# Optimization experiments

Hardware: AMD Instinct MI355X
Metric: run time of the kernel (lower is better)

The kernel has to match this reference:

```python
import jax, jax.numpy as jnp
import numpy as np

B, IN, OUT, K = 2048, 1024, 1024, 20


def setup_inputs() -> dict:
    key = jax.random.key(0)
    k1, k2 = jax.random.split(key)
    x = jax.random.normal(k1, (B, IN), dtype=jnp.float32)
    # per-output, per-input spline coefficients: (out_features, in_features, num_knots)
    W = jax.random.normal(k2, (OUT, IN, K), dtype=jnp.float32) * 0.1
    # evenly spaced knot grid on [-2, 2] (linspace)
    knots = jnp.linspace(-2.0, 2.0, K, dtype=jnp.float32)
    return {"x": x, "W": W, "knots": knots}


def reference(x, W, knots):
    # RBF spline basis shared across all output features (this is the fusion
    # the original per-output Python loop misses):
    # basis[b, i, k] = exp(-0.5 * ((x[b, i] - knots[k]) / h)^2)
    h = knots[1] - knots[0]  # uniform knot spacing -> RBF bandwidth
    basis = jnp.exp(-0.5 * jnp.square((x[:, :, None] - knots) / h))  # (B, IN, K)
    # Each SplineLayer o computes sum_{i,k} W[o,i,k] * basis[b,i,k]; the
    # KANBlock concatenates the OUT scalars -> a single einsum.
    return jnp.einsum("bik,oik->bo", basis, W)  # (B, OUT)
```

## Files before the change

### kernel.cpp

```cpp
#include <hip/hip_runtime.h>

#define B_DIM 2048
#define IN_DIM 1024
#define OUT_DIM 1024
#define K_KNOTS 20
#define KR (IN_DIM * K_KNOTS)
#define TM 128
#define TN 128
#define BK 64
#define KSPLIT 4
#define KPB (KR / KSPLIT)
#define OUT_ELEMS (B_DIM * OUT_DIM)
#define MT_TILES (B_DIM / TM)
#define NT_TILES (OUT_DIM / TN)
#define GEMM_BLOCKS (MT_TILES * NT_TILES * KSPLIT)

#define NB_PAIRS (B_DIM * IN_DIM * K_KNOTS / 2)
#define NB_BASIS_BLK (NB_PAIRS / 256)
#define NW4 (OUT_DIM * KR / 8)
#define NB_W_BLK (NW4 / 256)

typedef __bf16 bf16x8 __attribute__((ext_vector_type(8)));
typedef float  f32x4  __attribute__((ext_vector_type(4)));

__device__ __forceinline__ unsigned short f2bf(float f) {
    unsigned int u = __float_as_uint(f);
    unsigned int r = u + 0x7fffu + ((u >> 16) & 1u);
    return (unsigned short)(r >> 16);
}

__device__ __forceinline__ unsigned int pack2(float lo, float hi) {
    return (unsigned int)f2bf(lo) | ((unsigned int)f2bf(hi) << 16);
}

__device__ __forceinline__ void async_load16(const void* g, void* l) {
    __builtin_amdgcn_global_load_lds(
        (const __attribute__((address_space(1))) void*)g,
        (__attribute__((address_space(3))) void*)l,
        16, 0, 0);
}

__global__ void zero_out_kernel(float* out) {
    int idx = (blockIdx.x * 256 + threadIdx.x) * 4;
    float4 z = {0.f, 0.f, 0.f, 0.f};
    *(float4*)(out + idx) = z;
}

__global__ void prep_kernel(const float* __restrict__ x,
                            const float4* __restrict__ Wsrc,
                            const float* __restrict__ knots,
                            unsigned int* __restrict__ basis_out,
                            uint4* __restrict__ w_out) {
    if (blockIdx.x < NB_BASIS_BLK) {
        unsigned int n = blockIdx.x * 256 + threadIdx.x;
        unsigned int p  = n % 10u;
        unsigned int bi = n / 10u;
        float xv   = x[bi];
        float invh = 1.0f / (knots[1] - knots[0]);
        float t0 = knots[2 * p], t1 = knots[2 * p + 1];
        float d0 = (xv - t0) * invh;
        float d1 = (xv - t1) * invh;
        float v0 = __expf(-0.5f * d0 * d0);
        float v1 = __expf(-0.5f * d1 * d1);
        basis_out[n] = pack2(v0, v1);
    } else {
        unsigned int t = (blockIdx.x - NB_BASIS_BLK) * 256 + threadIdx.x;
        float4 a = Wsrc[2 * t];
        float4 b = Wsrc[2 * t + 1];
        uint4 o;
        o.x = pack2(a.x, a.y);
        o.y = pack2(a.z, a.w);
        o.z = pack2(b.x, b.y);
        o.w = pack2(b.z, b.w);
        w_out[t] = o;
    }
}

template <int KS, bool ATOMIC>
__global__ void __launch_bounds__(256)
kan_gemm(const unsigned short* __restrict__ Ab,
         const unsigned short* __restrict__ Bb,
         float* __restrict__ out) {
    __shared__ __align__(16) unsigned short As[TM * BK];
    __shared__ __align__(16) unsigned short Bs[TN * BK];

    const int KPBk = KR / KS;
    const int id   = blockIdx.x;
    const int xcd  = id & 7;
    const int ord  = id >> 3;
    const int mt   = xcd * 2 + (ord & 1);
    const int nt   = (ord >> 1) & (NT_TILES - 1);
    const int z    = ord >> (1 + 3);
    const int m0 = mt * TM;
    const int n0 = nt * TN;
    const int k0 = z * KPBk;

    const int tid  = threadIdx.x;
    const int wave = tid >> 6;
    const int lane = tid & 63;
    const int wm = wave & 1;
    const int wn = wave >> 1;

    const int srow = lane >> 3;
    const int scol = ((lane & 7) ^ srow) * 8;

    f32x4 acc[4][4];
#pragma unroll
    for (int i = 0; i < 4; ++i)
#pragma unroll
        for (int j = 0; j < 4; ++j) acc[i][j] = (f32x4){0.f, 0.f, 0.f, 0.f};

    for (int kt = 0; kt < KPBk; kt += BK) {
        const int kb = k0 + kt;
        __syncthreads();
#pragma unroll
        for (int c = 0; c < 4; ++c) {
            const int chunk = wave * 4 + c;
            const int r = chunk * 8 + srow;
            async_load16(Ab + (size_t)(m0 + r) * KR + kb + scol, &As[chunk * 512]);
            async_load16(Bb + (size_t)(n0 + r) * KR + kb + scol, &Bs[chunk * 512]);
        }
        __syncthreads();

        const int quad = lane >> 4;
        const int r15  = lane & 15;
        const int r7   = lane & 7;
#pragma unroll
        for (int s = 0; s < 2; ++s) {
            const int cg = s * 4 + quad;
            const int xo = (cg ^ r7) * 8;
            bf16x8 af[4], bfv[4];
#pragma unroll
            for (int i = 0; i < 4; ++i) {
                af[i]  = *(const bf16x8*)&As[(wm * 64 + i * 16 + r15) * BK + xo];
                bfv[i] = *(const bf16x8*)&Bs[(wn * 64 + i * 16 + r15) * BK + xo];
            }
#pragma unroll
            for (int i = 0; i < 4; ++i)
#pragma unroll
                for (int j = 0; j < 4; ++j)
                    acc[i][j] = __builtin_amdgcn_mfma_f32_16x16x32_bf16(
                        af[i], bfv[j], acc[i][j], 0, 0, 0);
        }
    }

    float* dst = ATOMIC ? out : out + (size_t)z * OUT_ELEMS;
    const int quad = lane >> 4;
    const int col  = lane & 15;
#pragma unroll
    for (int i = 0; i < 4; ++i)
#pragma unroll
        for (int j = 0; j < 4; ++j)
#pragma unroll
            for (int r = 0; r < 4; ++r) {
                const int row = m0 + wm * 64 + i * 16 + quad * 4 + r;
                const int c   = n0 + wn * 64 + j * 16 + col;
                if (ATOMIC)
                    atomicAdd(&dst[(size_t)row * OUT_DIM + c], acc[i][j][r]);
                else
                    dst[(size_t)row * OUT_DIM + c] = acc[i][j][r];
            }
}

template <int KS>
__global__ void kan_reduce(const float* __restrict__ part, float* __restrict__ out) {
    const int idx = (blockIdx.x * 256 + threadIdx.x) * 4;
    f32x4 s = *(const f32x4*)(part + idx);
#pragma unroll
    for (int z = 1; z < KS; ++z)
        s += *(const f32x4*)(part + (size_t)z * OUT_ELEMS + idx);
    *(f32x4*)(out + idx) = s;
}

__global__ void kan_fallback(const float* __restrict__ x,
                             const float* __restrict__ W,
                             const float* __restrict__ knots,
                             float* __restrict__ out) {
    __shared__ float basis[256 * K_KNOTS];
    const int b = blockIdx.x;
    const int o = blockIdx.y * blockDim.x + threadIdx.x;
    const float invh = 1.0f / (knots[1] - knots[0]);
    const float* w = W + (size_t)o * KR;
    float sum = 0.f;
    for (int i0 = 0; i0 < IN_DIM; i0 += 256) {
        __syncthreads();
        for (int idx = threadIdx.x; idx < 256 * K_KNOTS; idx += blockDim.x) {
            const int i = i0 + idx / K_KNOTS;
            const int k = idx % K_KNOTS;
            const float d = (x[(size_t)b * IN_DIM + i] - knots[k]) * invh;
            basis[idx] = __expf(-0.5f * d * d);
        }
        __syncthreads();
        for (int r = 0; r < 256 * K_KNOTS; ++r)
            sum += basis[r] * w[(size_t)i0 * K_KNOTS + r];
    }
    out[(size_t)b * OUT_DIM + o] = sum;
}

extern "C" void kernel_launch(void* const* d_in, const int* in_sizes, int n_in,
                              void* d_out, int out_size, void* d_ws, size_t ws_size,
                              hipStream_t stream) {
    const float* x     = (const float*)d_in[0];
    const float* W     = (const float*)d_in[1];
    const float* knots = (const float*)d_in[2];
    float* out = (float*)d_out;

    const size_t basis_bytes = (size_t)B_DIM * KR * 2;
    const size_t wb_bytes    = (size_t)OUT_DIM * KR * 2;
    const size_t part_bytes  = (size_t)KSPLIT * OUT_ELEMS * 4;

    unsigned short* Ab = (unsigned short*)d_ws;
    unsigned short* Bb = (unsigned short*)((char*)d_ws + basis_bytes);
    float* part = (float*)((char*)d_ws + basis_bytes + wb_bytes);

    if (ws_size >= basis_bytes + wb_bytes + part_bytes) {
        prep_kernel<<<dim3(NB_BASIS_BLK + NB_W_BLK), dim3(256), 0, stream>>>(
            x, (const float4*)W, knots, (unsigned int*)Ab, (uint4*)Bb);
        kan_gemm<KSPLIT, false><<<dim3(GEMM_BLOCKS), dim3(256), 0, stream>>>(Ab, Bb, part);
        kan_reduce<KSPLIT><<<dim3(OUT_ELEMS / (256 * 4)), dim3(256), 0, stream>>>(part, out);
    } else if (ws_size >= basis_bytes + wb_bytes) {
        zero_out_kernel<<<dim3(OUT_ELEMS / (256 * 4)), dim3(256), 0, stream>>>(out);
        prep_kernel<<<dim3(NB_BASIS_BLK + NB_W_BLK), dim3(256), 0, stream>>>(
            x, (const float4*)W, knots, (unsigned int*)Ab, (uint4*)Bb);
        kan_gemm<KSPLIT, true><<<dim3(GEMM_BLOCKS), dim3(256), 0, stream>>>(Ab, Bb, out);
    } else {
        kan_fallback<<<dim3(B_DIM, OUT_DIM / 256), dim3(256), 0, stream>>>(x, W, knots, out);
    }
}
```

Baseline: 285.3 us.

## Double GEMM K-tile to 128 and compute four basis values per thread

Raises the GEMM K-step from 64 to 128, so each block loads a 128x128 bf16 A and B tile per iteration and runs four MFMA sub-steps between barriers. The LDS swizzle and load mapping are reworked to match, and shared memory per block doubles. The prep kernel now computes four RBF basis values per thread with 8-byte stores, and rebuilds the knots from the first knot and the spacing instead of reading each one. This halves the number of barrier/sync rounds in the GEMM and reduces per-thread overhead in prep, at the cost of higher LDS use that may reduce occupancy.

```diff
diff --git a/kernel.cpp b/kernel.cpp
--- a/kernel.cpp
+++ b/kernel.cpp
@@ -7,7 +7,7 @@
 #define KR (IN_DIM * K_KNOTS)
 #define TM 128
 #define TN 128
-#define BK 64
+#define BK 128
 #define KSPLIT 4
 #define KPB (KR / KSPLIT)
 #define OUT_ELEMS (B_DIM * OUT_DIM)
@@ -15,8 +15,8 @@
 #define NT_TILES (OUT_DIM / TN)
 #define GEMM_BLOCKS (MT_TILES * NT_TILES * KSPLIT)
 
-#define NB_PAIRS (B_DIM * IN_DIM * K_KNOTS / 2)
-#define NB_BASIS_BLK (NB_PAIRS / 256)
+#define NB_QUADS (B_DIM * IN_DIM * 5)
+#define NB_BASIS_BLK (NB_QUADS / 256)
 #define NW4 (OUT_DIM * KR / 8)
 #define NB_W_BLK (NW4 / 256)
 
@@ -46,23 +46,32 @@
     *(float4*)(out + idx) = z;
 }
 
-__global__ void prep_kernel(const float* __restrict__ x,
-                            const float4* __restrict__ Wsrc,
-                            const float* __restrict__ knots,
-                            unsigned int* __restrict__ basis_out,
-                            uint4* __restrict__ w_out) {
+__global__ void __launch_bounds__(256) prep_kernel(
+        const float* __restrict__ x,
+        const float4* __restrict__ Wsrc,
+        const float* __restrict__ knots,
+        uint2* __restrict__ basis_out,
+        uint4* __restrict__ w_out) {
     if (blockIdx.x < NB_BASIS_BLK) {
         unsigned int n = blockIdx.x * 256 + threadIdx.x;
-        unsigned int p  = n % 10u;
-        unsigned int bi = n / 10u;
-        float xv   = x[bi];
-        float invh = 1.0f / (knots[1] - knots[0]);
-        float t0 = knots[2 * p], t1 = knots[2 * p + 1];
-        float d0 = (xv - t0) * invh;
-        float d1 = (xv - t1) * invh;
-        float v0 = __expf(-0.5f * d0 * d0);
-        float v1 = __expf(-0.5f * d1 * d1);
-        basis_out[n] = pack2(v0, v1);
+        unsigned int q  = n % 5u;
+        unsigned int bi = n / 5u;
+        float t0 = knots[0];
+        float h  = knots[1] - t0;
+        float invh = 1.0f / h;
+        float xv = x[bi];
+        float k0 = (float)(4 * q);
+        float v[4];
+#pragma unroll
+        for (int j = 0; j < 4; ++j) {
+            float t = __builtin_fmaf(k0 + (float)j, h, t0);
+            float d = (xv - t) * invh;
+            v[j] = __expf(-0.5f * d * d);
+        }
+        uint2 o;
+        o.x = pack2(v[0], v[1]);
+        o.y = pack2(v[2], v[3]);
+        basis_out[n] = o;
     } else {
         unsigned int t = (blockIdx.x - NB_BASIS_BLK) * 256 + threadIdx.x;
         float4 a = Wsrc[2 * t];
@@ -90,7 +99,7 @@
     const int ord  = id >> 3;
     const int mt   = xcd * 2 + (ord & 1);
     const int nt   = (ord >> 1) & (NT_TILES - 1);
-    const int z    = ord >> (1 + 3);
+    const int z    = ord >> 4;
     const int m0 = mt * TM;
     const int n0 = nt * TN;
     const int k0 = z * KPBk;
@@ -101,8 +110,8 @@
     const int wm = wave & 1;
     const int wn = wave >> 1;
 
-    const int srow = lane >> 3;
-    const int scol = ((lane & 7) ^ srow) * 8;
+    const int srow = lane >> 4;
+    const int sslot = lane & 15;
 
     f32x4 acc[4][4];
 #pragma unroll
@@ -114,11 +123,12 @@
         const int kb = k0 + kt;
         __syncthreads();
 #pragma unroll
-        for (int c = 0; c < 4; ++c) {
-            const int chunk = wave * 4 + c;
-            const int r = chunk * 8 + srow;
-            async_load16(Ab + (size_t)(m0 + r) * KR + kb + scol, &As[chunk * 512]);
-            async_load16(Bb + (size_t)(n0 + r) * KR + kb + scol, &Bs[chunk * 512]);
+        for (int c = 0; c < 8; ++c) {
+            const int chunk = wave * 8 + c;
+            const int r = chunk * 4 + srow;
+            const int gcol = ((sslot ^ (r & 7)) * 8);
+            async_load16(Ab + (size_t)(m0 + r) * KR + kb + gcol, &As[chunk * 512]);
+            async_load16(Bb + (size_t)(n0 + r) * KR + kb + gcol, &Bs[chunk * 512]);
         }
         __syncthreads();
 
@@ -126,9 +136,9 @@
         const int r15  = lane & 15;
         const int r7   = lane & 7;
 #pragma unroll
-        for (int s = 0; s < 2; ++s) {
-            const int cg = s * 4 + quad;
-            const int xo = (cg ^ r7) * 8;
+        for (int s = 0; s < 4; ++s) {
+            const int g  = s * 4 + quad;
+            const int xo = (g ^ r7) * 8;
             bf16x8 af[4], bfv[4];
 #pragma unroll
             for (int i = 0; i < 4; ++i) {
@@ -215,13 +225,13 @@
 
     if (ws_size >= basis_bytes + wb_bytes + part_bytes) {
         prep_kernel<<<dim3(NB_BASIS_BLK + NB_W_BLK), dim3(256), 0, stream>>>(
-            x, (const float4*)W, knots, (unsigned int*)Ab, (uint4*)Bb);
+            x, (const float4*)W, knots, (uint2*)Ab, (uint4*)Bb);
         kan_gemm<KSPLIT, false><<<dim3(GEMM_BLOCKS), dim3(256), 0, stream>>>(Ab, Bb, part);
         kan_reduce<KSPLIT><<<dim3(OUT_ELEMS / (256 * 4)), dim3(256), 0, stream>>>(part, out);
     } else if (ws_size >= basis_bytes + wb_bytes) {
         zero_out_kernel<<<dim3(OUT_ELEMS / (256 * 4)), dim3(256), 0, stream>>>(out);
         prep_kernel<<<dim3(NB_BASIS_BLK + NB_W_BLK), dim3(256), 0, stream>>>(
-            x, (const float4*)W, knots, (unsigned int*)Ab, (uint4*)Bb);
+            x, (const float4*)W, knots, (uint2*)Ab, (uint4*)Bb);
         kan_gemm<KSPLIT, true><<<dim3(GEMM_BLOCKS), dim3(256), 0, stream>>>(Ab, Bb, out);
     } else {
         kan_fallback<<<dim3(B_DIM, OUT_DIM / 256), dim3(256), 0, stream>>>(x, W, knots, out);
```

After: 260.9 us. 1.09x faster.
